# Performance work log

Hardware: AMD Instinct MI355X
Metric: run time of the kernel (lower is better)

The kernel has to match this reference:

```python
import jax, jax.numpy as jnp
import numpy as np

B, S, D = 2, 2048, 2048
H, DN, DR, DV = 16, 128, 64, 128   # heads, qk_nope, qk_rope, v_head
Q_LORA, KV_LORA = 1536, 512
DQ = DN + DR                        # qk_head_dim = 192
EPS = 1e-6


def setup_inputs() -> dict:
    key = jax.random.key(0)
    ks = jax.random.split(key, 8)
    s = 0.02  # weight init scale
    hidden_states = jax.random.normal(ks[0], (B, S, D), jnp.float32)
    # RoPE tables (non-interleaved HF style: cat(freqs, freqs)) per position
    inv_freq = 1.0 / (10000.0 ** (np.arange(0, DR, 2, dtype=np.float32) / DR))
    freqs = np.arange(S, dtype=np.float32)[:, None] * inv_freq[None, :]  # [S, DR/2]
    emb = np.concatenate([freqs, freqs], axis=-1)                        # [S, DR]
    cos = jnp.broadcast_to(jnp.asarray(np.cos(emb)), (B, S, DR))
    sin = jnp.broadcast_to(jnp.asarray(np.sin(emb)), (B, S, DR))
    return {
        'hidden_states': hidden_states,
        'cos': cos, 'sin': sin,
        'Wqa': jax.random.normal(ks[1], (D, Q_LORA), jnp.float32) * s,
        'qa_ln_w': jnp.ones((Q_LORA,), jnp.float32),
        'Wqb': jax.random.normal(ks[2], (Q_LORA, H * DQ), jnp.float32) * s,
        'Wkva': jax.random.normal(ks[3], (D, KV_LORA + DR), jnp.float32) * s,
        'kva_ln_w': jnp.ones((KV_LORA,), jnp.float32),
        'Wkvb': jax.random.normal(ks[4], (KV_LORA, H * (DN + DV)), jnp.float32) * s,
        'Wo': jax.random.normal(ks[5], (H * DV, D), jnp.float32) * s,
    }


def _rmsnorm(x, w):
    xf = x.astype(jnp.float32)
    var = jnp.mean(xf * xf, axis=-1, keepdims=True)
    return w * (xf * jax.lax.rsqrt(var + EPS)).astype(x.dtype)


def _rotate_half(x):
    h = x.shape[-1] // 2
    return jnp.concatenate([-x[..., h:], x[..., :h]], axis=-1)


def reference(hidden_states, cos, sin, Wqa, qa_ln_w, Wqb, Wkva, kva_ln_w, Wkvb, Wo):
    b, s, _ = hidden_states.shape
    scaling = DQ ** -0.5

    # Q path: down-proj -> RMSNorm -> up-proj -> [b, H, s, DQ]
    q = _rmsnorm(hidden_states @ Wqa, qa_ln_w) @ Wqb
    q = q.reshape(b, s, H, DQ).transpose(0, 2, 1, 3)
    q_pass, q_rot = q[..., :DN], q[..., DN:]

    # KV path: joint down-proj -> split latent / shared rope key
    ckv = hidden_states @ Wkva                       # [b, s, KV_LORA + DR]
    k_lat, k_rot = ckv[..., :KV_LORA], ckv[..., KV_LORA:]
    kv = _rmsnorm(k_lat, kva_ln_w) @ Wkvb            # [b, s, H*(DN+DV)]
    kv = kv.reshape(b, s, H, DN + DV).transpose(0, 2, 1, 3)
    k_pass, v = kv[..., :DN], kv[..., DN:]

    # decoupled RoPE on q_rot and the single shared k_rot head
    k_rot = k_rot[:, None, :, :]                     # [b, 1, s, DR]
    c, si = cos[:, None], sin[:, None]               # unsqueeze_dim=1
    q_rot = q_rot * c + _rotate_half(q_rot) * si
    k_rot = k_rot * c + _rotate_half(k_rot) * si
    k_rot = jnp.broadcast_to(k_rot, (b, H, s, DR))

    Q = jnp.concatenate([q_pass, q_rot], axis=-1)    # [b, H, s, DQ]
    K = jnp.concatenate([k_pass, k_rot], axis=-1)

    scores = jnp.einsum('bhqd,bhkd->bhqk', Q, K) * scaling
    neg = jnp.finfo(jnp.float32).min
    causal = jnp.where(jnp.tril(jnp.ones((s, s), bool)), 0.0, neg)
    scores = scores + causal
    w = jax.nn.softmax(scores.astype(jnp.float32), axis=-1).astype(Q.dtype)

    out = jnp.einsum('bhqk,bhkd->bhqd', w, v)
    out = out.transpose(0, 2, 1, 3).reshape(b, s, H * DV)
    return out @ Wo
```

## Files before the change

### kernel.cpp

```cpp
#include <hip/hip_runtime.h>
#include <math.h>

#define BB 2
#define SS 2048
#define DD 2048
#define HH 16
#define DN 128
#define DR 64
#define DV 128
#define QL 1536
#define KVL 512
#define DQ 192
#define CKVS 640
#define KVD 256
#define NCAT 2176
#define NCATP 2304
#define EPSF 1e-6f

typedef short bfrag __attribute__((ext_vector_type(8)));
typedef float facc  __attribute__((ext_vector_type(4)));

__device__ __forceinline__ ushort f2bf(float f) {
    union { float f; unsigned u; } v; v.f = f;
    unsigned r = v.u + 0x7fffu + ((v.u >> 16) & 1u);
    return (ushort)(r >> 16);
}
__device__ __forceinline__ float bf2f(ushort u) {
    union { unsigned u; float f; } v; v.u = ((unsigned)u) << 16;
    return v.f;
}
__device__ __forceinline__ float wave_red_sum(float v) {
    #pragma unroll
    for (int o = 32; o > 0; o >>= 1) v += __shfl_down(v, o);
    return v;
}
__device__ __forceinline__ void gl2lds16(const ushort* g, ushort* l) {
    __builtin_amdgcn_global_load_lds(
        (const __attribute__((address_space(1))) void*)g,
        (__attribute__((address_space(3))) void*)l, 16, 0, 0);
}
__device__ __forceinline__ void storeC(float* c, float v)  { *c = v; }
__device__ __forceinline__ void storeC(ushort* c, float v) { *c = f2bf(v); }

__global__ __launch_bounds__(256) void castf2bf(const float* __restrict__ x,
                                                ushort* __restrict__ y) {
    const int i = blockIdx.x * 256 + threadIdx.x;
    const float4 v = ((const float4*)x)[i];
    ushort4 o;
    o.x = f2bf(v.x); o.y = f2bf(v.y); o.z = f2bf(v.z); o.w = f2bf(v.w);
    ((ushort4*)y)[i] = o;
}

struct WtBatch {
    const float* src[5];
    ushort* dst[5];
    int K[5];
    int N[5];
    int nx[5];
    int base[6];
};
__global__ __launch_bounds__(256) void wtrans_b(WtBatch d) {
    __shared__ float tile[32][33];
    int bid = blockIdx.x;
    int seg = 0;
    while (bid >= d.base[seg + 1]) ++seg;
    const int l = bid - d.base[seg];
    const int nx = d.nx[seg];
    const int bx = l % nx, by = l / nx;
    const float* W = d.src[seg];
    ushort* Wt = d.dst[seg];
    const int K = d.K[seg], N = d.N[seg];
    const int k0 = by * 32, n0 = bx * 32;
    const int t = threadIdx.x;
    const int tx = t & 31, ty = t >> 5;
    #pragma unroll
    for (int r = 0; r < 4; ++r) {
        const int n = n0 + tx;
        tile[ty + r * 8][tx] =
            (n < N) ? W[(size_t)(k0 + ty + r * 8) * N + n] : 0.f;
    }
    __syncthreads();
    #pragma unroll
    for (int r = 0; r < 4; ++r) {
        const int n = n0 + ty + r * 8;
        Wt[(size_t)n * K + k0 + tx] = f2bf(tile[tx][ty + r * 8]);
    }
}


__device__ __forceinline__ void stage_half(const ushort* __restrict__ G,
                                           int ldg, int grow0, int kcol0,
                                           ushort* Lr, int wave, int lane) {
    const int r0   = lane >> 3;
    const int slot = (lane & 7) ^ r0;
    const ushort* s0 = G + (size_t)(grow0 + wave * 16 + r0) * ldg + kcol0 + slot * 8;
    gl2lds16(s0,                    Lr + wave * 1024);
    gl2lds16(s0 + (size_t)8 * ldg,  Lr + wave * 1024 + 512);
}

#define PH_PRE  do { __builtin_amdgcn_sched_barrier(0);                      \
                     __builtin_amdgcn_s_barrier();                           \
                     asm volatile("s_waitcnt lgkmcnt(0)" ::: "memory");      \
                     __builtin_amdgcn_sched_barrier(0);                      \
                     __builtin_amdgcn_s_setprio(1); } while (0)
#define PH_POST do { __builtin_amdgcn_s_setprio(0);                          \
                     __builtin_amdgcn_sched_barrier(0);                      \
                     __builtin_amdgcn_s_barrier(); } while (0)

#define MFMA16(RB)                                                           \
    _Pragma("unroll")                                                        \
    for (int i = 0; i < 4; ++i)                                              \
        _Pragma("unroll")                                                    \
        for (int j = 0; j < 4; ++j)                                          \
            acc[(RB) + i][j] = __builtin_amdgcn_mfma_f32_16x16x32_bf16(      \
                a[i], b[j], acc[(RB) + i][j], 0, 0, 0);

#define GEMM256_CORE(A_, Bt_, K_, NBX_)                                       \
    __shared__ ushort L[65536];                           \
    const int t    = threadIdx.x;                                             \
    const int lane = t & 63;                                                  \
    const int wave = t >> 6;                                                  \
    const int wm   = wave >> 2;                                               \
    const int wn   = wave & 3;                                                \
    const int quad = lane >> 4;                                               \
    const int lrow = lane & 15;                                               \
    int wg = (int)blockIdx.x;                                                 \
    { const int cpx = (int)gridDim.x >> 3; wg = (wg & 7) * cpx + (wg >> 3); } \
    const int bx = wg % (NBX_), by = wg / (NBX_);                             \
    const int m0 = by * 256, n0 = bx * 256;                                   \
    const int s0x8  = (quad ^ (lrow & 7)) * 8;       \
    const int s1x8  = s0x8 ^ 32;                   \
    const int abase = lrow * 64;                                              \
    const int bbase = (wn & 1) * 4096 + lrow * 64;                            \
    facc acc[8][4];                                                           \
    _Pragma("unroll")                                                         \
    for (int i = 0; i < 8; ++i)                                               \
        _Pragma("unroll")                                                     \
        for (int j = 0; j < 4; ++j) acc[i][j] = (facc)(0.f);                  \
    const int nk = (K_) >> 6;                                                 \
                  \
    stage_half((A_),  (K_), m0,        0, L,         wave, lane);             \
    stage_half((A_),  (K_), m0 + 128,  0, L + 8192,  wave, lane);             \
    stage_half((Bt_), (K_), n0,        0, L + 16384, wave, lane);             \
    stage_half((Bt_), (K_), n0 + 128,  0, L + 24576, wave, lane);             \
    stage_half((Bt_), (K_), n0,       64, L + 49152, wave, lane);             \
    stage_half((Bt_), (K_), n0 + 128, 64, L + 57344, wave, lane);             \
    asm volatile("s_waitcnt vmcnt(4)" ::: "memory");                          \
    __builtin_amdgcn_s_barrier();                                             \
    for (int kt = 0; kt < nk; ++kt) {                                         \
        const int p = kt & 1;                                                 \
        ushort* LA = L + p * 32768 + wm * 8192;                               \
        ushort* LB = L + p * 32768 + 16384 + (wn >> 1) * 8192;                \
        ushort* Lq = L + (p ^ 1) * 32768;                                     \
        const int kn = (kt + 1) * 64;                                         \
        bfrag a[4], b[4];                                                     \
                                           \
        _Pragma("unroll")                                                     \
        for (int i = 0; i < 4; ++i)                                           \
            a[i] = *(const bfrag*)(LA + i * 1024 + abase + s0x8);             \
        _Pragma("unroll")                                                     \
        for (int j = 0; j < 4; ++j)                                           \
            b[j] = *(const bfrag*)(LB + bbase + j * 1024 + s0x8);             \
        if (kt + 1 < nk) stage_half((A_), (K_), m0, kn, Lq, wave, lane);      \
        PH_PRE;                                                               \
        MFMA16(0)                                                             \
        PH_POST;                                                              \
                                \
        _Pragma("unroll")                                                     \
        for (int i = 0; i < 4; ++i)                                           \
            a[i] = *(const bfrag*)(LA + (4 + i) * 1024 + abase + s0x8);       \
        if (kt + 1 < nk)                                                      \
            stage_half((A_), (K_), m0 + 128, kn, Lq + 8192, wave, lane);      \
        PH_PRE;                                                               \
        MFMA16(4)                                                             \
        PH_POST;                                                              \
                                           \
        _Pragma("unroll")                                                     \
        for (int i = 0; i < 4; ++i)                                           \
            a[i] = *(const bfrag*)(LA + i * 1024 + abase + s1x8);             \
        _Pragma("unroll")                                                     \
        for (int j = 0; j < 4; ++j)                                           \
            b[j] = *(const bfrag*)(LB + bbase + j * 1024 + s1x8);             \
        PH_PRE;                                                               \
        MFMA16(0)                                                             \
        PH_POST;                                                              \
             \
        _Pragma("unroll")                                                     \
        for (int i = 0; i < 4; ++i)                                           \
            a[i] = *(const bfrag*)(LA + (4 + i) * 1024 + abase + s1x8);       \
        if (kt + 2 < nk) {                                                    \
            stage_half((Bt_), (K_), n0,       kn + 64,                        \
                       L + p * 32768 + 16384, wave, lane);                    \
            stage_half((Bt_), (K_), n0 + 128, kn + 64,                        \
                       L + p * 32768 + 24576, wave, lane);                    \
            asm volatile("s_waitcnt vmcnt(4)" ::: "memory");                  \
        } else {                                                              \
            asm volatile("s_waitcnt vmcnt(0)" ::: "memory");                  \
        }                                                                     \
        PH_PRE;                                                               \
        MFMA16(4)                                                             \
        PH_POST;                                                              \
    }

template <typename OUT, int K, int NBX, int NOUT>
__global__ __launch_bounds__(512, 2) void gemm256(const ushort* __restrict__ A,
                                                  const ushort* __restrict__ Bt,
                                                  OUT* __restrict__ C) {
    GEMM256_CORE(A, Bt, K, NBX)
    #pragma unroll
    for (int m = 0; m < 8; ++m) {
        const int row = m0 + wm * 128 + m * 16 + quad * 4;
        #pragma unroll
        for (int nf = 0; nf < 4; ++nf) {
            const int col = n0 + wn * 64 + nf * 16 + lrow;
            #pragma unroll
            for (int r = 0; r < 4; ++r)
                storeC(&C[(size_t)(row + r) * NOUT + col], acc[m][nf][r]);
        }
    }
}

__global__ __launch_bounds__(512, 2) void gemmA256(const ushort* __restrict__ A,
                                                   const ushort* __restrict__ Bt,
                                                   ushort* __restrict__ qa,
                                                   ushort* __restrict__ ckv) {
    GEMM256_CORE(A, Bt, DD, 9)
    #pragma unroll
    for (int m = 0; m < 8; ++m) {
        const int row = m0 + wm * 128 + m * 16 + quad * 4;
        #pragma unroll
        for (int nf = 0; nf < 4; ++nf) {
            const int col = n0 + wn * 64 + nf * 16 + lrow;
            #pragma unroll
            for (int r = 0; r < 4; ++r) {
                if (col < QL)
                    qa[(size_t)(row + r) * QL + col] = f2bf(acc[m][nf][r]);
                else if (col < NCAT)
                    ckv[(size_t)(row + r) * CKVS + col - QL] = f2bf(acc[m][nf][r]);
            }
        }
    }
}

__global__ __launch_bounds__(512, 2) void gemmQ256(const ushort* __restrict__ A,
                                                   const ushort* __restrict__ Bt,
                                                   ushort* __restrict__ Qbuf) {
    GEMM256_CORE(A, Bt, QL, 12)
    const float scaling = 0.07216878364870323f;
    #pragma unroll
    for (int m = 0; m < 8; ++m) {
        const int row = m0 + wm * 128 + m * 16 + quad * 4;
        #pragma unroll
        for (int nf = 0; nf < 4; ++nf) {
            const int col = n0 + wn * 64 + nf * 16 + lrow;
            const int h = col / DQ, d = col - h * DQ;
            #pragma unroll
            for (int r = 0; r < 4; ++r) {
                const int tok = row + r;
                const int b = tok >> 11, s = tok & (SS - 1);
                Qbuf[((size_t)(b * HH + h) * SS + s) * DQ + d] =
                    f2bf(acc[m][nf][r] * scaling);
            }
        }
    }
}

__global__ __launch_bounds__(256) void rmsnorm_bf_ip(ushort* __restrict__ x,
                                                     const float* __restrict__ w,
                                                     int n) {
    ushort* xr = x + (size_t)blockIdx.x * n;
    const int t = threadIdx.x;
    float ss = 0.f;
    for (int i = t; i < n; i += 256) { float v = bf2f(xr[i]); ss += v * v; }
    ss = wave_red_sum(ss);
    __shared__ float red[4];
    const int lane = t & 63, wid = t >> 6;
    if (lane == 0) red[wid] = ss;
    __syncthreads();
    const float tot = red[0] + red[1] + red[2] + red[3];
    const float scale = rsqrtf(tot / (float)n + EPSF);
    for (int i = t; i < n; i += 256) xr[i] = f2bf(w[i] * bf2f(xr[i]) * scale);
}

__global__ __launch_bounds__(256) void rmsnorm_kv(const ushort* __restrict__ x,
                                                  const float* __restrict__ w,
                                                  ushort* __restrict__ y,
                                                  ushort* __restrict__ krb,
                                                  const float* __restrict__ cosb,
                                                  const float* __restrict__ sinb) {
    const int row = blockIdx.x;
    const ushort* xr = x + (size_t)row * CKVS;
    ushort* yr = y + (size_t)row * KVL;
    const int t = threadIdx.x;
    if (t < 64) {
        const int p = t;
        const ushort* kin = xr + KVL;
        const float c  = cosb[(size_t)row * DR + p];
        const float sn = sinb[(size_t)row * DR + p];
        const float self = bf2f(kin[p]);
        const float partner = bf2f(kin[p < 32 ? p + 32 : p - 32]);
        const float v = (p < 32) ? (self * c - partner * sn)
                                 : (self * c + partner * sn);
        krb[(size_t)row * DR + p] = f2bf(v);
    }
    float ss = 0.f;
    for (int i = t; i < KVL; i += 256) { float v = bf2f(xr[i]); ss += v * v; }
    ss = wave_red_sum(ss);
    __shared__ float red[4];
    const int lane = t & 63, wid = t >> 6;
    if (lane == 0) red[wid] = ss;
    __syncthreads();
    const float tot = red[0] + red[1] + red[2] + red[3];
    const float scale = rsqrtf(tot / (float)KVL + EPSF);
    for (int i = t; i < KVL; i += 256) yr[i] = f2bf(w[i] * bf2f(xr[i]) * scale);
}

__global__ __launch_bounds__(256) void qrope(ushort* __restrict__ Qbuf,
                                             const float* __restrict__ cosb,
                                             const float* __restrict__ sinb) {
    const int tok = blockIdx.x;
    const int b = tok >> 11, s = tok & (SS - 1);
    const int t = threadIdx.x;
    const int p = t & 31, hh = t >> 5;
    const float c0 = cosb[(size_t)tok * DR + p];
    const float s0 = sinb[(size_t)tok * DR + p];
    const float c1 = cosb[(size_t)tok * DR + p + 32];
    const float s1 = sinb[(size_t)tok * DR + p + 32];
    #pragma unroll
    for (int it = 0; it < 2; ++it) {
        const int h = hh + it * 8;
        ushort* base = Qbuf + ((size_t)(b * HH + h) * SS + s) * DQ + DN;
        const float x0 = bf2f(base[p]), x1 = bf2f(base[p + 32]);
        base[p]      = f2bf(x0 * c0 - x1 * s0);
        base[p + 32] = f2bf(x1 * c1 + x0 * s1);
    }
}

__global__ __launch_bounds__(256) void vprep(const ushort* __restrict__ kv_bf,
                                             ushort* __restrict__ Vtb) {
    __shared__ ushort tile[32][33];
    const int kp0 = blockIdx.x * 32, dv0 = blockIdx.y * 32, bh = blockIdx.z;
    const int b = bh / HH, h = bh - b * HH;
    const int t = threadIdx.x, tx = t & 31, ty = t >> 5;
    #pragma unroll
    for (int r = 0; r < 4; ++r)
        tile[ty + r * 8][tx] =
            kv_bf[(size_t)(b * SS + kp0 + ty + r * 8) * (HH * KVD) + h * KVD + DN + dv0 + tx];
    __syncthreads();
    #pragma unroll
    for (int r = 0; r < 4; ++r)
        Vtb[((size_t)bh * DV + dv0 + ty + r * 8) * SS + kp0 + tx] = tile[tx][ty + r * 8];
}

__global__ __launch_bounds__(256, 2) void fattn_mfma(
    const ushort* __restrict__ Qb,
    const ushort* __restrict__ kvb,
    const ushort* __restrict__ krb,
    const ushort* __restrict__ Vt,
    ushort* __restrict__ o)
{
    const int h  = blockIdx.y;
    const int b  = blockIdx.z;
    const int qt = b ? (15 - (int)blockIdx.x) : (int)blockIdx.x;
    const int bh = b * HH + h;
    const int q0 = qt * 128;
    const int t    = threadIdx.x;
    const int lane = t & 63;
    const int wave = t >> 6;
    const int quad = lane >> 4;
    const int n    = lane & 15;
    const int wstrip = wave * 16;

    __shared__ ushort Ksu[6 * 64 * 32];
    __shared__ ushort Vtu[2 * 128 * 32];
    __shared__ ushort Psu[2 * 128 * 40];

    const ushort* vbase = Vt + (size_t)bh * DV * SS;

    bfrag aQ[2][6];
    #pragma unroll
    for (int sp = 0; sp < 2; ++sp) {
        const ushort* qrow = Qb + ((size_t)bh * SS + q0 + sp * 64 + wstrip + n) * DQ;
        #pragma unroll
        for (int kb = 0; kb < 6; ++kb)
            aQ[sp][kb] = *(const bfrag*)(qrow + kb * 32 + quad * 8);
    }

    facc oacc[2][8];
    float lp[2][4];
    #pragma unroll
    for (int sp = 0; sp < 2; ++sp) {
        #pragma unroll
        for (int jd = 0; jd < 8; ++jd) oacc[sp][jd] = (facc)(0.f);
        #pragma unroll
        for (int r = 0; r < 4; ++r) lp[sp][r] = 0.f;
    }

    const int nkt = 2 * qt + 2;
    for (int kt = 0; kt < nkt; ++kt) {
        const int k0 = kt * 64;

        #pragma unroll
        for (int i = 0; i < 6; ++i) {
            const int g = wave + 4 * i;
            const int kb = g >> 2;
            const int rem = (g & 3) * 64 + lane;
            const int row = rem >> 2, sub = rem & 3;
            const int tok = b * SS + k0 + row;
            const ushort* src = (kb < 4)
                ? kvb + (size_t)tok * (HH * KVD) + h * KVD + kb * 32 + sub * 8
                : krb + (size_t)tok * DR + (kb - 4) * 32 + sub * 8;
            gl2lds16(src, Ksu + g * 512);
        }
        #pragma unroll
        for (int i = 0; i < 4; ++i) {
            const int g = wave + 4 * i;
            const int kb2 = g >> 3;
            const int rem = (g & 7) * 64 + lane;
            const int dv = rem >> 2, sub = rem & 3;
            gl2lds16(vbase + (size_t)dv * SS + k0 + kb2 * 32 + sub * 8,
                     Vtu + g * 512);
        }
        __syncthreads();

        facc s[2][4];
        #pragma unroll
        for (int sp = 0; sp < 2; ++sp)
            #pragma unroll
            for (int j = 0; j < 4; ++j) s[sp][j] = (facc)(0.f);
        #pragma unroll
        for (int kb = 0; kb < 6; ++kb) {
            #pragma unroll
            for (int j = 0; j < 4; ++j) {
                const bfrag bk =
                    *(const bfrag*)&Ksu[kb * 2048 + (j * 16 + n) * 32 + quad * 8];
                s[0][j] = __builtin_amdgcn_mfma_f32_16x16x32_bf16(aQ[0][kb], bk, s[0][j], 0, 0, 0);
                s[1][j] = __builtin_amdgcn_mfma_f32_16x16x32_bf16(aQ[1][kb], bk, s[1][j], 0, 0, 0);
            }
        }

        #pragma unroll
        for (int sp = 0; sp < 2; ++sp) {
            const int rowg0 = q0 + sp * 64 + wstrip + quad * 4;
            #pragma unroll
            for (int j = 0; j < 4; ++j) {
                const int kpos = k0 + j * 16 + n;
                #pragma unroll
                for (int r = 0; r < 4; ++r) {
                    float p = (kpos <= rowg0 + r) ? __expf(s[sp][j][r]) : 0.f;
                    lp[sp][r] += p;
                    Psu[(j >> 1) * 5120 + (sp * 64 + wstrip + quad * 4 + r) * 40
                        + (j & 1) * 16 + n] = f2bf(p);
                }
            }
        }

        #pragma unroll
        for (int kb2 = 0; kb2 < 2; ++kb2) {
            const bfrag aP0 = *(const bfrag*)&Psu[kb2 * 5120 + (wstrip + n) * 40 + quad * 8];
            const bfrag aP1 = *(const bfrag*)&Psu[kb2 * 5120 + (64 + wstrip + n) * 40 + quad * 8];
            #pragma unroll
            for (int jd = 0; jd < 8; ++jd) {
                const bfrag bV = *(const bfrag*)&Vtu[kb2 * 4096 + (jd * 16 + n) * 32 + quad * 8];
                oacc[0][jd] = __builtin_amdgcn_mfma_f32_16x16x32_bf16(aP0, bV, oacc[0][jd], 0, 0, 0);
                oacc[1][jd] = __builtin_amdgcn_mfma_f32_16x16x32_bf16(aP1, bV, oacc[1][jd], 0, 0, 0);
            }
        }
        __syncthreads();
    }

    #pragma unroll
    for (int sp = 0; sp < 2; ++sp) {
        #pragma unroll
        for (int r = 0; r < 4; ++r) {
            float v = lp[sp][r];
            #pragma unroll
            for (int msk = 1; msk < 16; msk <<= 1) v += __shfl_xor(v, msk);
            const float inv = 1.f / v;
            ushort* op = o + (size_t)(b * SS + q0 + sp * 64 + wstrip + quad * 4 + r)
                             * (HH * DV) + h * DV;
            #pragma unroll
            for (int jd = 0; jd < 8; ++jd)
                op[jd * 16 + n] = f2bf(oacc[sp][jd][r] * inv);
        }
    }
}

extern "C" void kernel_launch(void* const* d_in, const int* in_sizes, int n_in,
                              void* d_out, int out_size, void* d_ws, size_t ws_size,
                              hipStream_t stream) {
    const float* hs    = (const float*)d_in[0];
    const float* cosb  = (const float*)d_in[1];
    const float* sinb  = (const float*)d_in[2];
    const float* Wqa   = (const float*)d_in[3];
    const float* qa_w  = (const float*)d_in[4];
    const float* Wqb   = (const float*)d_in[5];
    const float* Wkva  = (const float*)d_in[6];
    const float* kva_w = (const float*)d_in[7];
    const float* Wkvb  = (const float*)d_in[8];
    const float* Wo    = (const float*)d_in[9];
    float* out = (float*)d_out;

    const int T = BB * SS;

    char* w = (char*)d_ws;
    auto alloc = [&](size_t bytes) {
        void* r = (void*)w;
        w += (bytes + 255) & ~(size_t)255;
        return r;
    };
    ushort* hs_bf  = (ushort*)alloc((size_t)T * DD * 2);
    ushort* Wcat   = (ushort*)alloc((size_t)NCATP * DD * 2);
    ushort* Wqbt   = (ushort*)alloc((size_t)(HH * DQ) * QL * 2);
    ushort* Wkvbt  = (ushort*)alloc((size_t)(HH * KVD) * KVL * 2);
    ushort* Wot    = (ushort*)alloc((size_t)DD * DD * 2);
    ushort* qa_bf  = (ushort*)alloc((size_t)T * QL * 2);
    ushort* Qbuf   = (ushort*)alloc((size_t)T * HH * DQ * 2);
    ushort* ckv_bf = (ushort*)alloc((size_t)T * CKVS * 2);
    ushort* kvn_bf = (ushort*)alloc((size_t)T * KVL * 2);
    ushort* kv_bf  = (ushort*)alloc((size_t)T * HH * KVD * 2);
    ushort* krb    = (ushort*)alloc((size_t)T * DR * 2);
    ushort* Vtb    = Wcat;
    ushort* ao_bf  = hs_bf;

    castf2bf<<<(T * DD / 4) / 256, 256, 0, stream>>>(hs, hs_bf);
    WtBatch wb;
    wb.src[0] = Wqa;  wb.dst[0] = Wcat;                      wb.K[0] = DD;  wb.N[0] = QL;       wb.nx[0] = 48;
    wb.src[1] = Wkva; wb.dst[1] = Wcat + (size_t)QL * DD;    wb.K[1] = DD;  wb.N[1] = KVL + DR; wb.nx[1] = 20;
    wb.src[2] = Wqb;  wb.dst[2] = Wqbt;                      wb.K[2] = QL;  wb.N[2] = HH * DQ;  wb.nx[2] = 96;
    wb.src[3] = Wkvb; wb.dst[3] = Wkvbt;                     wb.K[3] = KVL; wb.N[3] = HH * KVD; wb.nx[3] = 128;
    wb.src[4] = Wo;   wb.dst[4] = Wot;                       wb.K[4] = DD;  wb.N[4] = DD;       wb.nx[4] = 64;
    wb.base[0] = 0;
    wb.base[1] = wb.base[0] + wb.nx[0] * (DD / 32);
    wb.base[2] = wb.base[1] + wb.nx[1] * (DD / 32);
    wb.base[3] = wb.base[2] + wb.nx[2] * (QL / 32);
    wb.base[4] = wb.base[3] + wb.nx[3] * (KVL / 32);
    wb.base[5] = wb.base[4] + wb.nx[4] * (DD / 32);
    wtrans_b<<<wb.base[5], 256, 0, stream>>>(wb);

    gemmA256<<<dim3(9 * 16), 512, 0, stream>>>(hs_bf, Wcat, qa_bf, ckv_bf);
    rmsnorm_bf_ip<<<T, 256, 0, stream>>>(qa_bf, qa_w, QL);
    gemmQ256<<<dim3(12 * 16), 512, 0, stream>>>(qa_bf, Wqbt, Qbuf);
    qrope<<<T, 256, 0, stream>>>(Qbuf, cosb, sinb);
    rmsnorm_kv<<<T, 256, 0, stream>>>(ckv_bf, kva_w, kvn_bf, krb, cosb, sinb);
    gemm256<ushort, KVL, 16, HH * KVD><<<dim3(16 * 16), 512, 0, stream>>>(kvn_bf, Wkvbt, kv_bf);
    vprep<<<dim3(SS / 32, DV / 32, BB * HH), 256, 0, stream>>>(kv_bf, Vtb);
    fattn_mfma<<<dim3(16, HH, BB), 256, 0, stream>>>(Qbuf, kv_bf, krb, Vtb, ao_bf);
    gemm256<float, DD, 8, DD><<<dim3(8 * 16), 512, 0, stream>>>(ao_bf, Wot, out);
}
```

Measured before the change: 451.3 us.

## Prefetch next K/V tile into registers during attention compute

The attention loop now loads the first K/V tile before the loop. Inside the loop it issues global loads for the next tile into registers while the current tile's QK and PV MFMAs run, then writes those registers to LDS after a barrier. This hides global-memory latency behind compute at the cost of extra VGPRs, which may lower occupancy. It also adds a fast path that skips causal mask comparisons on tiles that lie fully below the diagonal.

```diff
diff --git a/kernel.cpp b/kernel.cpp
--- a/kernel.cpp
+++ b/kernel.cpp
@@ -396,32 +396,57 @@
         for (int r = 0; r < 4; ++r) lp[sp][r] = 0.f;
     }
 
+    #pragma unroll
+    for (int i = 0; i < 6; ++i) {
+        const int g = wave + 4 * i;
+        const int kb = g >> 2;
+        const int rem = (g & 3) * 64 + lane;
+        const int row = rem >> 2, sub = rem & 3;
+        const int tok = b * SS + row;
+        const ushort* src = (kb < 4)
+            ? kvb + (size_t)tok * (HH * KVD) + h * KVD + kb * 32 + sub * 8
+            : krb + (size_t)tok * DR + (kb - 4) * 32 + sub * 8;
+        gl2lds16(src, Ksu + g * 512);
+    }
+    #pragma unroll
+    for (int i = 0; i < 4; ++i) {
+        const int g = wave + 4 * i;
+        const int kb2 = g >> 3;
+        const int rem = (g & 7) * 64 + lane;
+        const int dv = rem >> 2, sub = rem & 3;
+        gl2lds16(vbase + (size_t)dv * SS + kb2 * 32 + sub * 8, Vtu + g * 512);
+    }
+    __syncthreads();
+
     const int nkt = 2 * qt + 2;
     for (int kt = 0; kt < nkt; ++kt) {
         const int k0 = kt * 64;
-
-        #pragma unroll
-        for (int i = 0; i < 6; ++i) {
-            const int g = wave + 4 * i;
-            const int kb = g >> 2;
-            const int rem = (g & 3) * 64 + lane;
-            const int row = rem >> 2, sub = rem & 3;
-            const int tok = b * SS + k0 + row;
-            const ushort* src = (kb < 4)
-                ? kvb + (size_t)tok * (HH * KVD) + h * KVD + kb * 32 + sub * 8
-                : krb + (size_t)tok * DR + (kb - 4) * 32 + sub * 8;
-            gl2lds16(src, Ksu + g * 512);
-        }
-        #pragma unroll
-        for (int i = 0; i < 4; ++i) {
-            const int g = wave + 4 * i;
-            const int kb2 = g >> 3;
-            const int rem = (g & 7) * 64 + lane;
-            const int dv = rem >> 2, sub = rem & 3;
-            gl2lds16(vbase + (size_t)dv * SS + k0 + kb2 * 32 + sub * 8,
-                     Vtu + g * 512);
-        }
-        __syncthreads();
+        const int k1 = k0 + 64;
+        const bool more = (kt + 1 < nkt);
+
+        bfrag kreg[6], vreg[4];
+        if (more) {
+            #pragma unroll
+            for (int i = 0; i < 6; ++i) {
+                const int g = wave + 4 * i;
+                const int kb = g >> 2;
+                const int rem = (g & 3) * 64 + lane;
+                const int row = rem >> 2, sub = rem & 3;
+                const int tok = b * SS + k1 + row;
+                const ushort* src = (kb < 4)
+                    ? kvb + (size_t)tok * (HH * KVD) + h * KVD + kb * 32 + sub * 8
+                    : krb + (size_t)tok * DR + (kb - 4) * 32 + sub * 8;
+                kreg[i] = *(const bfrag*)src;
+            }
+            #pragma unroll
+            for (int i = 0; i < 4; ++i) {
+                const int g = wave + 4 * i;
+                const int kb2 = g >> 3;
+                const int rem = (g & 7) * 64 + lane;
+                const int dv = rem >> 2, sub = rem & 3;
+                vreg[i] = *(const bfrag*)(vbase + (size_t)dv * SS + k1 + kb2 * 32 + sub * 8);
+            }
+        }
 
         facc s[2][4];
         #pragma unroll
@@ -439,18 +464,35 @@
             }
         }
 
-        #pragma unroll
-        for (int sp = 0; sp < 2; ++sp) {
-            const int rowg0 = q0 + sp * 64 + wstrip + quad * 4;
-            #pragma unroll
-            for (int j = 0; j < 4; ++j) {
-                const int kpos = k0 + j * 16 + n;
+        const bool fullt = (k1 <= q0);
+        if (fullt) {
+            #pragma unroll
+            for (int sp = 0; sp < 2; ++sp) {
                 #pragma unroll
-                for (int r = 0; r < 4; ++r) {
-                    float p = (kpos <= rowg0 + r) ? __expf(s[sp][j][r]) : 0.f;
-                    lp[sp][r] += p;
-                    Psu[(j >> 1) * 5120 + (sp * 64 + wstrip + quad * 4 + r) * 40
-                        + (j & 1) * 16 + n] = f2bf(p);
+                for (int j = 0; j < 4; ++j) {
+                    #pragma unroll
+                    for (int r = 0; r < 4; ++r) {
+                        const float p = __expf(s[sp][j][r]);
+                        lp[sp][r] += p;
+                        Psu[(j >> 1) * 5120 + (sp * 64 + wstrip + quad * 4 + r) * 40
+                            + (j & 1) * 16 + n] = f2bf(p);
+                    }
+                }
+            }
+        } else {
+            #pragma unroll
+            for (int sp = 0; sp < 2; ++sp) {
+                const int rowg0 = q0 + sp * 64 + wstrip + quad * 4;
+                #pragma unroll
+                for (int j = 0; j < 4; ++j) {
+                    const int kpos = k0 + j * 16 + n;
+                    #pragma unroll
+                    for (int r = 0; r < 4; ++r) {
+                        const float p = (kpos <= rowg0 + r) ? __expf(s[sp][j][r]) : 0.f;
+                        lp[sp][r] += p;
+                        Psu[(j >> 1) * 5120 + (sp * 64 + wstrip + quad * 4 + r) * 40
+                            + (j & 1) * 16 + n] = f2bf(p);
+                    }
                 }
             }
         }
@@ -465,6 +507,16 @@
                 oacc[0][jd] = __builtin_amdgcn_mfma_f32_16x16x32_bf16(aP0, bV, oacc[0][jd], 0, 0, 0);
                 oacc[1][jd] = __builtin_amdgcn_mfma_f32_16x16x32_bf16(aP1, bV, oacc[1][jd], 0, 0, 0);
             }
+        }
+
+        __syncthreads();
+        if (more) {
+            #pragma unroll
+            for (int i = 0; i < 6; ++i)
+                *(bfrag*)(Ksu + (wave + 4 * i) * 512 + lane * 8) = kreg[i];
+            #pragma unroll
+            for (int i = 0; i < 4; ++i)
+                *(bfrag*)(Vtu + (wave + 4 * i) * 512 + lane * 8) = vreg[i];
         }
         __syncthreads();
     }
```

After: 449.0 us. About the same (-0.5%).
